# Kernel tuning notes

Hardware: AMD Instinct MI355X
Metric: run time of the kernel (lower is better)

The kernel has to match this reference:

```python
import jax, jax.numpy as jnp
import numpy as np

TEMPERATURE = 8.0  # sqrt(head_dim=64)
NEG_FILL = -1000000000.0

def setup_inputs() -> dict:
    key = jax.random.key(0)
    k1, k2, k3, k4, k5 = jax.random.split(key, 5)
    B, H, S, D = 4, 16, 1024, 64
    q = jax.random.normal(k1, (B, H, S, D), dtype=jnp.float32)
    k = jax.random.normal(k2, (B, H, S, D), dtype=jnp.float32)
    v = jax.random.normal(k3, (B, H, S, D), dtype=jnp.float32)
    similarity = jax.random.normal(k4, (B, H, S, S), dtype=jnp.float32)
    mask = jax.random.randint(k5, (B, 1, S, S), 0, 2).astype(bool)
    return {"q": q, "k": k, "v": v, "similarity": similarity, "mask": mask}

def reference(q, k, v, similarity, mask):
    # scores: [B,H,S,S] = (q/temp) @ k^T
    attn = jnp.einsum('bhqd,bhkd->bhqk', q / TEMPERATURE, k)
    attn = jnp.where(mask, NEG_FILL, attn)          # masked_fill (mask broadcasts over heads)
    attn = jax.nn.softmax(attn + similarity, axis=-1)  # dropout p=0 (eval): identity
    output = jnp.einsum('bhqk,bhkd->bhqd', attn, v)
    return (output, attn)
```

## Files before the change

### kernel.cpp

```cpp
#include <hip/hip_runtime.h>
#include <stdint.h>


#define S_LEN 1024
#define D_DIM 64
#define QT 16
#define NEG_FILL (-1000000000.0f)
#define LOG2E 1.44269504088896340736f

typedef __bf16 bf16x8 __attribute__((ext_vector_type(8)));
typedef float f32x4 __attribute__((ext_vector_type(4)));
typedef unsigned short u16x4 __attribute__((ext_vector_type(4)));

__device__ __forceinline__ unsigned short f2bf(float x) {
    unsigned u = __builtin_bit_cast(unsigned, x);
    u += 0x7fffu + ((u >> 16) & 1u);
    return (unsigned short)(u >> 16);
}
__device__ __forceinline__ float bf2f(unsigned short b) {
    return __builtin_bit_cast(float, (unsigned)b << 16);
}

__device__ __forceinline__ unsigned short* sptr(unsigned short* s, int row, int col) {
    return (unsigned short*)((char*)s + row * 2048 + ((col * 2) ^ ((row & 7) << 4)));
}

__global__ void prep_qkm(const float* __restrict__ q, const float* __restrict__ k,
                         const void* __restrict__ mraw,
                         unsigned short* __restrict__ Qb, unsigned short* __restrict__ Kb,
                         unsigned char* __restrict__ Mb)
{
    const int t = threadIdx.x;
    const int i = blockIdx.x * 256 + t;
    f32x4 q4 = ((const f32x4*)q)[i];
    f32x4 k4 = ((const f32x4*)k)[i];
    u16x4 qo, ko;
#pragma unroll
    for (int j = 0; j < 4; ++j) {
        qo[j] = f2bf(q4[j] * 0.125f);
        ko[j] = f2bf(k4[j]);
    }
    ((u16x4*)Qb)[i] = qo;
    ((u16x4*)Kb)[i] = ko;

    __shared__ int s_not_int, s_not_f32;
    if (t == 0) { s_not_int = 0; s_not_f32 = 0; }
    __syncthreads();
    const unsigned* wdd = (const unsigned*)mraw;
    int ni = 0, nf = 0;
    for (int j = t; j < 1024; j += 256) {
        unsigned x = wdd[j];
        if (x > 1u) ni = 1;
        if (x != 0u && x != 0x3f800000u) nf = 1;
    }
    if (ni) s_not_int = 1;
    if (nf) s_not_f32 = 1;
    __syncthreads();
    const int fmt = (s_not_int == 0) ? 0 : ((s_not_f32 == 0) ? 1 : 2);
    uchar4 o;
    if (fmt == 0) {
        int4 x = ((const int4*)mraw)[i];
        o.x = x.x ? 1 : 0; o.y = x.y ? 1 : 0; o.z = x.z ? 1 : 0; o.w = x.w ? 1 : 0;
    } else if (fmt == 1) {
        float4 x = ((const float4*)mraw)[i];
        o.x = (x.x != 0.f) ? 1 : 0; o.y = (x.y != 0.f) ? 1 : 0;
        o.z = (x.z != 0.f) ? 1 : 0; o.w = (x.w != 0.f) ? 1 : 0;
    } else {
        uchar4 x = ((const uchar4*)mraw)[i];
        o.x = x.x ? 1 : 0; o.y = x.y ? 1 : 0; o.z = x.z ? 1 : 0; o.w = x.w ? 1 : 0;
    }
    ((uchar4*)Mb)[i] = o;
}

__global__ void prep_vt(const float* __restrict__ v, unsigned short* __restrict__ Vt)
{
    __shared__ unsigned short sT[64 * 72];
    const int bh = blockIdx.x >> 4;
    const int st = blockIdx.x & 15;
    const int t = threadIdx.x;
    const float* vb = v + (size_t)(bh * S_LEN + st * 64) * D_DIM;
#pragma unroll
    for (int p = 0; p < 4; ++p) {
        int lin = p * 256 + t;
        int r = lin >> 4;
        int c = lin & 15;
        f32x4 x = ((const f32x4*)(vb + r * D_DIM))[c];
        unsigned short* dst = &sT[r * 72 + c * 4];
#pragma unroll
        for (int j = 0; j < 4; ++j) dst[j] = f2bf(x[j]);
    }
    __syncthreads();
    unsigned short* ob = Vt + (size_t)bh * D_DIM * S_LEN + st * 64;
#pragma unroll
    for (int p = 0; p < 4; ++p) {
        int lin = p * 256 + t;
        int d = lin >> 4;
        int s4 = (lin & 15) * 4;
        u16x4 o;
#pragma unroll
        for (int j = 0; j < 4; ++j) o[j] = sT[(s4 + j) * 72 + d];
        *(u16x4*)&ob[d * S_LEN + s4] = o;
    }
}

__global__ __launch_bounds__(256, 5)
void attn_main(const float* __restrict__ simg_, const unsigned short* __restrict__ Qb,
               const unsigned short* __restrict__ Kb, const unsigned short* __restrict__ Vtb,
               const unsigned char* __restrict__ Mb, float* __restrict__ out,
               float* __restrict__ attn)
{
    __shared__ __align__(16) unsigned short sS[QT * S_LEN];

    const int blk = blockIdx.x;
    const int bh = blk >> 6;
    const int qt = blk & 63;
    const int b = bh >> 4;
    const int t = threadIdx.x;
    const int w = t >> 6;
    const int lane = t & 63;
    const int quad = lane >> 4;
    const int l15 = lane & 15;

    const unsigned short* Qg = Qb + (size_t)(bh * S_LEN + qt * QT) * D_DIM;
    const unsigned short* Kg = Kb + (size_t)bh * S_LEN * D_DIM;
    const unsigned short* Vg = Vtb + (size_t)bh * D_DIM * S_LEN;
    const float* simg = simg_ + ((size_t)(bh * S_LEN + qt * QT)) * S_LEN;
    const unsigned char* mg = Mb + ((size_t)(b * S_LEN + qt * QT)) * S_LEN;
    float* attng = attn + ((size_t)(bh * S_LEN + qt * QT)) * S_LEN;

    const int n0 = w * 16;
    const bf16x8 av0 = *(const bf16x8*)&Qg[l15 * D_DIM + quad * 8];
    const bf16x8 av1 = *(const bf16x8*)&Qg[l15 * D_DIM + 32 + quad * 8];
    const unsigned short* kp0 = &Kg[(size_t)(n0 + l15) * D_DIM + quad * 8];
    bf16x8 kb0 = *(const bf16x8*)kp0;
    bf16x8 kb1 = *(const bf16x8*)(kp0 + 32);
#pragma unroll 4
    for (int kt = 0; kt < 16; ++kt) {
        bf16x8 bv0 = kb0, bv1 = kb1;
        if (kt < 15) {
            const unsigned short* kp = &Kg[(size_t)((kt + 1) * 64 + n0 + l15) * D_DIM + quad * 8];
            kb0 = *(const bf16x8*)kp;
            kb1 = *(const bf16x8*)(kp + 32);
        }
        f32x4 acc = {0.f, 0.f, 0.f, 0.f};
        acc = __builtin_amdgcn_mfma_f32_16x16x32_bf16(av0, bv0, acc, 0, 0, 0);
        acc = __builtin_amdgcn_mfma_f32_16x16x32_bf16(av1, bv1, acc, 0, 0, 0);
        const int colg = kt * 64 + n0 + l15;
#pragma unroll
        for (int r = 0; r < 4; ++r)
            *sptr(sS, quad * 4 + r, colg) = f2bf(acc[r]);
    }

    const float* sp_w = simg + (size_t)(w * 4) * S_LEN;
    f32x4 svb[2][4];
#pragma unroll
    for (int j = 0; j < 4; ++j)
        svb[0][j] = __builtin_nontemporal_load((const f32x4*)&sp_w[j * 256 + lane * 4]);
    __syncthreads();

#pragma unroll
    for (int rr = 0; rr < 4; ++rr) {
        const int cb = rr & 1;
        const int row = w * 4 + rr;
        if (rr < 3) {
            const float* spn = sp_w + (size_t)(rr + 1) * S_LEN;
#pragma unroll
            for (int j = 0; j < 4; ++j)
                svb[cb ^ 1][j] = __builtin_nontemporal_load((const f32x4*)&spn[j * 256 + lane * 4]);
        }
        const unsigned char* mp = mg + (size_t)row * S_LEN;
        float vals[16];
        float mx = -3.0e38f;
#pragma unroll
        for (int j = 0; j < 4; ++j) {
            const int col = j * 256 + lane * 4;
            u16x4 x = *(const u16x4*)sptr(sS, row, col);
            uchar4 mk = *(const uchar4*)&mp[col];
            f32x4 sv = svb[cb][j];
            float f0 = mk.x ? NEG_FILL : (bf2f(x[0]) + sv[0]);
            float f1 = mk.y ? NEG_FILL : (bf2f(x[1]) + sv[1]);
            float f2 = mk.z ? NEG_FILL : (bf2f(x[2]) + sv[2]);
            float f3 = mk.w ? NEG_FILL : (bf2f(x[3]) + sv[3]);
            vals[j * 4 + 0] = f0; vals[j * 4 + 1] = f1;
            vals[j * 4 + 2] = f2; vals[j * 4 + 3] = f3;
            mx = fmaxf(mx, fmaxf(fmaxf(f0, f1), fmaxf(f2, f3)));
        }
#pragma unroll
        for (int off = 32; off > 0; off >>= 1)
            mx = fmaxf(mx, __shfl_xor(mx, off, 64));
        float sum = 0.f;
#pragma unroll
        for (int i = 0; i < 16; ++i) {
            float e = __builtin_amdgcn_exp2f((vals[i] - mx) * LOG2E);
            vals[i] = e;
            sum += e;
        }
#pragma unroll
        for (int off = 32; off > 0; off >>= 1)
            sum += __shfl_xor(sum, off, 64);
        const float rinv = 1.0f / sum;
#pragma unroll
        for (int j = 0; j < 4; ++j) {
            const int col = j * 256 + lane * 4;
            f32x4 p;
            u16x4 pb;
#pragma unroll
            for (int i = 0; i < 4; ++i) {
                float pi = vals[j * 4 + i] * rinv;
                p[i] = pi;
                pb[i] = f2bf(pi);
            }
            __builtin_nontemporal_store(p, (f32x4*)&attng[(size_t)row * S_LEN + col]);
            *(u16x4*)sptr(sS, row, col) = pb;
        }
    }

    const int d0 = w * 16;
    const unsigned short* vpp = &Vg[(size_t)(d0 + l15) * S_LEN + quad * 8];
    bf16x8 vb0 = *(const bf16x8*)vpp;
    bf16x8 vb1 = *(const bf16x8*)(vpp + 32);
    __syncthreads();

    f32x4 oacc = {0.f, 0.f, 0.f, 0.f};
#pragma unroll 4
    for (int kt = 0; kt < 16; ++kt) {
        bf16x8 bv0 = vb0, bv1 = vb1;
        if (kt < 15) {
            const unsigned short* vp = &Vg[(size_t)(d0 + l15) * S_LEN + (kt + 1) * 64 + quad * 8];
            vb0 = *(const bf16x8*)vp;
            vb1 = *(const bf16x8*)(vp + 32);
        }
        bf16x8 pa0 = *(const bf16x8*)sptr(sS, l15, kt * 64 + quad * 8);
        bf16x8 pa1 = *(const bf16x8*)sptr(sS, l15, kt * 64 + 32 + quad * 8);
        oacc = __builtin_amdgcn_mfma_f32_16x16x32_bf16(pa0, bv0, oacc, 0, 0, 0);
        oacc = __builtin_amdgcn_mfma_f32_16x16x32_bf16(pa1, bv1, oacc, 0, 0, 0);
    }
    float* og = out + ((size_t)(bh * S_LEN + qt * QT)) * D_DIM;
#pragma unroll
    for (int r = 0; r < 4; ++r) {
        const int row = quad * 4 + r;
        __builtin_nontemporal_store(oacc[r], &og[row * D_DIM + d0 + l15]);
    }
}

extern "C" void kernel_launch(void* const* d_in, const int* in_sizes, int n_in,
                              void* d_out, int out_size, void* d_ws, size_t ws_size,
                              hipStream_t stream)
{
    const float* q = (const float*)d_in[0];
    const float* k = (const float*)d_in[1];
    const float* v = (const float*)d_in[2];
    const float* sim = (const float*)d_in[3];
    const void* mask = d_in[4];
    float* out = (float*)d_out;
    float* attn = out + (size_t)4 * 16 * 1024 * 64;

    char* ws = (char*)d_ws;
    unsigned short* Qb = (unsigned short*)(ws + (size_t)0);
    unsigned short* Kb = (unsigned short*)(ws + ((size_t)8 << 20));
    unsigned short* Vt = (unsigned short*)(ws + ((size_t)16 << 20));
    unsigned char*  Mb = (unsigned char*)(ws + ((size_t)24 << 20));

    prep_qkm<<<4096, 256, 0, stream>>>(q, k, mask, Qb, Kb, Mb);
    prep_vt<<<1024, 256, 0, stream>>>(v, Vt);
    attn_main<<<4096, 256, 0, stream>>>(sim, Qb, Kb, Vt, Mb, out, attn);
}
```

Measured before the change: 576.9 us.

## Deepen K/V prefetch, batch softmax rows in pairs, remap blocks across XCDs

```diff
diff --git a/kernel.cpp b/kernel.cpp
--- a/kernel.cpp
+++ b/kernel.cpp
@@ -103,7 +103,75 @@
     }
 }
 
-__global__ __launch_bounds__(256, 5)
+__device__ __forceinline__ void softmax2(
+    unsigned short* sS, const int row0, const int lane,
+    f32x4 (&v0)[4], f32x4 (&v1)[4],
+    uchar4 (&k0)[4], uchar4 (&k1)[4],
+    float* __restrict__ a0, float* __restrict__ a1)
+{
+    u16x4 x0[4], x1[4];
+#pragma unroll
+    for (int j = 0; j < 4; ++j) {
+        const int col = j * 256 + lane * 4;
+        x0[j] = *(const u16x4*)sptr(sS, row0, col);
+        x1[j] = *(const u16x4*)sptr(sS, row0 + 1, col);
+    }
+    float mx0 = -3.0e38f, mx1 = -3.0e38f;
+#pragma unroll
+    for (int j = 0; j < 4; ++j) {
+        f32x4 a = v0[j], b = v1[j];
+        const uchar4 ka = k0[j], kb = k1[j];
+        a[0] = ka.x ? NEG_FILL : (bf2f(x0[j][0]) + a[0]);
+        a[1] = ka.y ? NEG_FILL : (bf2f(x0[j][1]) + a[1]);
+        a[2] = ka.z ? NEG_FILL : (bf2f(x0[j][2]) + a[2]);
+        a[3] = ka.w ? NEG_FILL : (bf2f(x0[j][3]) + a[3]);
+        b[0] = kb.x ? NEG_FILL : (bf2f(x1[j][0]) + b[0]);
+        b[1] = kb.y ? NEG_FILL : (bf2f(x1[j][1]) + b[1]);
+        b[2] = kb.z ? NEG_FILL : (bf2f(x1[j][2]) + b[2]);
+        b[3] = kb.w ? NEG_FILL : (bf2f(x1[j][3]) + b[3]);
+        v0[j] = a; v1[j] = b;
+        mx0 = fmaxf(mx0, fmaxf(fmaxf(a[0], a[1]), fmaxf(a[2], a[3])));
+        mx1 = fmaxf(mx1, fmaxf(fmaxf(b[0], b[1]), fmaxf(b[2], b[3])));
+    }
+#pragma unroll
+    for (int off = 32; off > 0; off >>= 1) {
+        mx0 = fmaxf(mx0, __shfl_xor(mx0, off, 64));
+        mx1 = fmaxf(mx1, __shfl_xor(mx1, off, 64));
+    }
+    float s0 = 0.f, s1 = 0.f;
+#pragma unroll
+    for (int j = 0; j < 4; ++j) {
+        f32x4 a = v0[j], b = v1[j];
+#pragma unroll
+        for (int i = 0; i < 4; ++i) {
+            a[i] = __builtin_amdgcn_exp2f((a[i] - mx0) * LOG2E);
+            b[i] = __builtin_amdgcn_exp2f((b[i] - mx1) * LOG2E);
+            s0 += a[i];
+            s1 += b[i];
+        }
+        v0[j] = a; v1[j] = b;
+    }
+#pragma unroll
+    for (int off = 32; off > 0; off >>= 1) {
+        s0 += __shfl_xor(s0, off, 64);
+        s1 += __shfl_xor(s1, off, 64);
+    }
+    const float r0 = 1.0f / s0, r1 = 1.0f / s1;
+#pragma unroll
+    for (int j = 0; j < 4; ++j) {
+        const int col = j * 256 + lane * 4;
+        f32x4 p0 = v0[j] * r0, p1 = v1[j] * r1;
+        u16x4 q0, q1;
+#pragma unroll
+        for (int i = 0; i < 4; ++i) { q0[i] = f2bf(p0[i]); q1[i] = f2bf(p1[i]); }
+        __builtin_nontemporal_store(p0, (f32x4*)(a0 + col));
+        __builtin_nontemporal_store(p1, (f32x4*)(a1 + col));
+        *(u16x4*)sptr(sS, row0, col) = q0;
+        *(u16x4*)sptr(sS, row0 + 1, col) = q1;
+    }
+}
+
+__global__ __launch_bounds__(256, 4)
 void attn_main(const float* __restrict__ simg_, const unsigned short* __restrict__ Qb,
                const unsigned short* __restrict__ Kb, const unsigned short* __restrict__ Vtb,
                const unsigned char* __restrict__ Mb, float* __restrict__ out,
@@ -111,7 +179,7 @@
 {
     __shared__ __align__(16) unsigned short sS[QT * S_LEN];
 
-    const int blk = blockIdx.x;
+    const int blk = ((blockIdx.x & 7) << 9) | (blockIdx.x >> 3);
     const int bh = blk >> 6;
     const int qt = blk & 63;
     const int b = bh >> 4;
@@ -131,116 +199,119 @@
     const int n0 = w * 16;
     const bf16x8 av0 = *(const bf16x8*)&Qg[l15 * D_DIM + quad * 8];
     const bf16x8 av1 = *(const bf16x8*)&Qg[l15 * D_DIM + 32 + quad * 8];
-    const unsigned short* kp0 = &Kg[(size_t)(n0 + l15) * D_DIM + quad * 8];
-    bf16x8 kb0 = *(const bf16x8*)kp0;
-    bf16x8 kb1 = *(const bf16x8*)(kp0 + 32);
-#pragma unroll 4
-    for (int kt = 0; kt < 16; ++kt) {
-        bf16x8 bv0 = kb0, bv1 = kb1;
-        if (kt < 15) {
-            const unsigned short* kp = &Kg[(size_t)((kt + 1) * 64 + n0 + l15) * D_DIM + quad * 8];
-            kb0 = *(const bf16x8*)kp;
-            kb1 = *(const bf16x8*)(kp + 32);
-        }
-        f32x4 acc = {0.f, 0.f, 0.f, 0.f};
-        acc = __builtin_amdgcn_mfma_f32_16x16x32_bf16(av0, bv0, acc, 0, 0, 0);
-        acc = __builtin_amdgcn_mfma_f32_16x16x32_bf16(av1, bv1, acc, 0, 0, 0);
-        const int colg = kt * 64 + n0 + l15;
-#pragma unroll
-        for (int r = 0; r < 4; ++r)
-            *sptr(sS, quad * 4 + r, colg) = f2bf(acc[r]);
+    const unsigned short* kfrag = Kg + (size_t)(n0 + l15) * D_DIM + quad * 8;
+
+#define SB __builtin_amdgcn_sched_barrier(0)
+#define LOADK(D0, D1, KT) do { \
+    const unsigned short* _p = kfrag + (size_t)(KT) * 4096; \
+    D0 = *(const bf16x8*)_p; D1 = *(const bf16x8*)(_p + 32); } while (0)
+#define QKSTEP(F0, F1, KT) do { \
+    f32x4 _acc = {0.f, 0.f, 0.f, 0.f}; \
+    _acc = __builtin_amdgcn_mfma_f32_16x16x32_bf16(av0, F0, _acc, 0, 0, 0); \
+    _acc = __builtin_amdgcn_mfma_f32_16x16x32_bf16(av1, F1, _acc, 0, 0, 0); \
+    const int _cg = (KT) * 64 + n0 + l15; \
+    *sptr(sS, quad * 4 + 0, _cg) = f2bf(_acc[0]); \
+    *sptr(sS, quad * 4 + 1, _cg) = f2bf(_acc[1]); \
+    *sptr(sS, quad * 4 + 2, _cg) = f2bf(_acc[2]); \
+    *sptr(sS, quad * 4 + 3, _cg) = f2bf(_acc[3]); } while (0)
+
+    {
+        bf16x8 ka0, ka1, kb0, kb1, kc0, kc1, kd0, kd1;
+        LOADK(ka0, ka1, 0); LOADK(kb0, kb1, 1); LOADK(kc0, kc1, 2); LOADK(kd0, kd1, 3);
+        SB;
+        QKSTEP(ka0, ka1, 0);  LOADK(ka0, ka1, 4);  SB;
+        QKSTEP(kb0, kb1, 1);  LOADK(kb0, kb1, 5);  SB;
+        QKSTEP(kc0, kc1, 2);  LOADK(kc0, kc1, 6);  SB;
+        QKSTEP(kd0, kd1, 3);  LOADK(kd0, kd1, 7);  SB;
+        QKSTEP(ka0, ka1, 4);  LOADK(ka0, ka1, 8);  SB;
+        QKSTEP(kb0, kb1, 5);  LOADK(kb0, kb1, 9);  SB;
+        QKSTEP(kc0, kc1, 6);  LOADK(kc0, kc1, 10); SB;
+        QKSTEP(kd0, kd1, 7);  LOADK(kd0, kd1, 11); SB;
+        QKSTEP(ka0, ka1, 8);  LOADK(ka0, ka1, 12); SB;
+        QKSTEP(kb0, kb1, 9);  LOADK(kb0, kb1, 13); SB;
+        QKSTEP(kc0, kc1, 10); LOADK(kc0, kc1, 14); SB;
+        QKSTEP(kd0, kd1, 11); LOADK(kd0, kd1, 15); SB;
+        QKSTEP(ka0, ka1, 12);
+        QKSTEP(kb0, kb1, 13);
+        QKSTEP(kc0, kc1, 14);
+        QKSTEP(kd0, kd1, 15);
     }
 
     const float* sp_w = simg + (size_t)(w * 4) * S_LEN;
-    f32x4 svb[2][4];
-#pragma unroll
-    for (int j = 0; j < 4; ++j)
-        svb[0][j] = __builtin_nontemporal_load((const f32x4*)&sp_w[j * 256 + lane * 4]);
-    __syncthreads();
-
-#pragma unroll
-    for (int rr = 0; rr < 4; ++rr) {
-        const int cb = rr & 1;
-        const int row = w * 4 + rr;
-        if (rr < 3) {
-            const float* spn = sp_w + (size_t)(rr + 1) * S_LEN;
-#pragma unroll
-            for (int j = 0; j < 4; ++j)
-                svb[cb ^ 1][j] = __builtin_nontemporal_load((const f32x4*)&spn[j * 256 + lane * 4]);
-        }
-        const unsigned char* mp = mg + (size_t)row * S_LEN;
-        float vals[16];
-        float mx = -3.0e38f;
-#pragma unroll
-        for (int j = 0; j < 4; ++j) {
-            const int col = j * 256 + lane * 4;
-            u16x4 x = *(const u16x4*)sptr(sS, row, col);
-            uchar4 mk = *(const uchar4*)&mp[col];
-            f32x4 sv = svb[cb][j];
-            float f0 = mk.x ? NEG_FILL : (bf2f(x[0]) + sv[0]);
-            float f1 = mk.y ? NEG_FILL : (bf2f(x[1]) + sv[1]);
-            float f2 = mk.z ? NEG_FILL : (bf2f(x[2]) + sv[2]);
-            float f3 = mk.w ? NEG_FILL : (bf2f(x[3]) + sv[3]);
-            vals[j * 4 + 0] = f0; vals[j * 4 + 1] = f1;
-            vals[j * 4 + 2] = f2; vals[j * 4 + 3] = f3;
-            mx = fmaxf(mx, fmaxf(fmaxf(f0, f1), fmaxf(f2, f3)));
-        }
-#pragma unroll
-        for (int off = 32; off > 0; off >>= 1)
-            mx = fmaxf(mx, __shfl_xor(mx, off, 64));
-        float sum = 0.f;
-#pragma unroll
-        for (int i = 0; i < 16; ++i) {
-            float e = __builtin_amdgcn_exp2f((vals[i] - mx) * LOG2E);
-            vals[i] = e;
-            sum += e;
-        }
-#pragma unroll
-        for (int off = 32; off > 0; off >>= 1)
-            sum += __shfl_xor(sum, off, 64);
-        const float rinv = 1.0f / sum;
-#pragma unroll
-        for (int j = 0; j < 4; ++j) {
-            const int col = j * 256 + lane * 4;
-            f32x4 p;
-            u16x4 pb;
-#pragma unroll
-            for (int i = 0; i < 4; ++i) {
-                float pi = vals[j * 4 + i] * rinv;
-                p[i] = pi;
-                pb[i] = f2bf(pi);
-            }
-            __builtin_nontemporal_store(p, (f32x4*)&attng[(size_t)row * S_LEN + col]);
-            *(u16x4*)sptr(sS, row, col) = pb;
-        }
-    }
+    const unsigned char* mp_w = mg + (size_t)(w * 4) * S_LEN;
+    f32x4 sA[4], sB[4], sC[4], sD[4];
+    uchar4 mA[4], mB[4], mC[4], mD[4];
+#pragma unroll
+    for (int j = 0; j < 4; ++j) {
+        const int col = j * 256 + lane * 4;
+        sA[j] = __builtin_nontemporal_load((const f32x4*)&sp_w[col]);
+        sB[j] = __builtin_nontemporal_load((const f32x4*)&sp_w[S_LEN + col]);
+        mA[j] = *(const uchar4*)&mp_w[col];
+        mB[j] = *(const uchar4*)&mp_w[S_LEN + col];
+    }
+    SB;
+    __syncthreads();
+
+#pragma unroll
+    for (int j = 0; j < 4; ++j) {
+        const int col = j * 256 + lane * 4;
+        sC[j] = __builtin_nontemporal_load((const f32x4*)&sp_w[2 * S_LEN + col]);
+        sD[j] = __builtin_nontemporal_load((const f32x4*)&sp_w[3 * S_LEN + col]);
+        mC[j] = *(const uchar4*)&mp_w[2 * S_LEN + col];
+        mD[j] = *(const uchar4*)&mp_w[3 * S_LEN + col];
+    }
+    SB;
+    softmax2(sS, w * 4 + 0, lane, sA, sB, mA, mB,
+             attng + (size_t)(w * 4 + 0) * S_LEN, attng + (size_t)(w * 4 + 1) * S_LEN);
+    softmax2(sS, w * 4 + 2, lane, sC, sD, mC, mD,
+             attng + (size_t)(w * 4 + 2) * S_LEN, attng + (size_t)(w * 4 + 3) * S_LEN);
 
     const int d0 = w * 16;
-    const unsigned short* vpp = &Vg[(size_t)(d0 + l15) * S_LEN + quad * 8];
-    bf16x8 vb0 = *(const bf16x8*)vpp;
-    bf16x8 vb1 = *(const bf16x8*)(vpp + 32);
+    const unsigned short* vfrag = Vg + (size_t)(d0 + l15) * S_LEN + quad * 8;
+
+#define LOADV(D0, D1, KT) do { \
+    const unsigned short* _p = vfrag + (KT) * 64; \
+    D0 = *(const bf16x8*)_p; D1 = *(const bf16x8*)(_p + 32); } while (0)
+#define PVSTEP(F0, F1, KT) do { \
+    bf16x8 _pa0 = *(const bf16x8*)sptr(sS, l15, (KT) * 64 + quad * 8); \
+    bf16x8 _pa1 = *(const bf16x8*)sptr(sS, l15, (KT) * 64 + 32 + quad * 8); \
+    oacc = __builtin_amdgcn_mfma_f32_16x16x32_bf16(_pa0, F0, oacc, 0, 0, 0); \
+    oacc = __builtin_amdgcn_mfma_f32_16x16x32_bf16(_pa1, F1, oacc, 0, 0, 0); } while (0)
+
+    bf16x8 va0, va1, vb0, vb1, vc0, vc1, vd0, vd1;
+    LOADV(va0, va1, 0); LOADV(vb0, vb1, 1); LOADV(vc0, vc1, 2); LOADV(vd0, vd1, 3);
+    SB;
     __syncthreads();
 
     f32x4 oacc = {0.f, 0.f, 0.f, 0.f};
-#pragma unroll 4
-    for (int kt = 0; kt < 16; ++kt) {
-        bf16x8 bv0 = vb0, bv1 = vb1;
-        if (kt < 15) {
-            const unsigned short* vp = &Vg[(size_t)(d0 + l15) * S_LEN + (kt + 1) * 64 + quad * 8];
-            vb0 = *(const bf16x8*)vp;
-            vb1 = *(const bf16x8*)(vp + 32);
-        }
-        bf16x8 pa0 = *(const bf16x8*)sptr(sS, l15, kt * 64 + quad * 8);
-        bf16x8 pa1 = *(const bf16x8*)sptr(sS, l15, kt * 64 + 32 + quad * 8);
-        oacc = __builtin_amdgcn_mfma_f32_16x16x32_bf16(pa0, bv0, oacc, 0, 0, 0);
-        oacc = __builtin_amdgcn_mfma_f32_16x16x32_bf16(pa1, bv1, oacc, 0, 0, 0);
-    }
+    PVSTEP(va0, va1, 0);  LOADV(va0, va1, 4);  SB;
+    PVSTEP(vb0, vb1, 1);  LOADV(vb0, vb1, 5);  SB;
+    PVSTEP(vc0, vc1, 2);  LOADV(vc0, vc1, 6);  SB;
+    PVSTEP(vd0, vd1, 3);  LOADV(vd0, vd1, 7);  SB;
+    PVSTEP(va0, va1, 4);  LOADV(va0, va1, 8);  SB;
+    PVSTEP(vb0, vb1, 5);  LOADV(vb0, vb1, 9);  SB;
+    PVSTEP(vc0, vc1, 6);  LOADV(vc0, vc1, 10); SB;
+    PVSTEP(vd0, vd1, 7);  LOADV(vd0, vd1, 11); SB;
+    PVSTEP(va0, va1, 8);  LOADV(va0, va1, 12); SB;
+    PVSTEP(vb0, vb1, 9);  LOADV(vb0, vb1, 13); SB;
+    PVSTEP(vc0, vc1, 10); LOADV(vc0, vc1, 14); SB;
+    PVSTEP(vd0, vd1, 11); LOADV(vd0, vd1, 15); SB;
+    PVSTEP(va0, va1, 12);
+    PVSTEP(vb0, vb1, 13);
+    PVSTEP(vc0, vc1, 14);
+    PVSTEP(vd0, vd1, 15);
+
     float* og = out + ((size_t)(bh * S_LEN + qt * QT)) * D_DIM;
 #pragma unroll
     for (int r = 0; r < 4; ++r) {
         const int row = quad * 4 + r;
         __builtin_nontemporal_store(oacc[r], &og[row * D_DIM + d0 + l15]);
     }
+#undef SB
+#undef LOADK
+#undef QKSTEP
+#undef LOADV
+#undef PVSTEP
 }
 
 extern "C" void kernel_launch(void* const* d_in, const int* in_sizes, int n_in,
```

Result: no change. 570.5 us (-1.1%).

## Pipeline K/V loads four deep with explicit vmcnt waits and swizzle block order

Applied to the files above, without the earlier changes.

```diff
diff --git a/kernel.cpp b/kernel.cpp
--- a/kernel.cpp
+++ b/kernel.cpp
@@ -20,6 +20,20 @@
 __device__ __forceinline__ float bf2f(unsigned short b) {
     return __builtin_bit_cast(float, (unsigned)b << 16);
 }
+
+__device__ __forceinline__ f32x4 gload16(const void* p) {
+    f32x4 d;
+    asm volatile("global_load_dwordx4 %0, %1, off" : "=v"(d) : "v"(p) : "memory");
+    return d;
+}
+__device__ __forceinline__ unsigned gload4(const void* p) {
+    unsigned d;
+    asm volatile("global_load_dword %0, %1, off" : "=v"(d) : "v"(p) : "memory");
+    return d;
+}
+#define WAITV(N) do { \
+    asm volatile("s_waitcnt vmcnt(" #N ")" ::: "memory"); \
+    __builtin_amdgcn_sched_barrier(0); } while (0)
 
 __device__ __forceinline__ unsigned short* sptr(unsigned short* s, int row, int col) {
     return (unsigned short*)((char*)s + row * 2048 + ((col * 2) ^ ((row & 7) << 4)));
@@ -103,7 +117,7 @@
     }
 }
 
-__global__ __launch_bounds__(256, 5)
+__global__ __launch_bounds__(256, 4)
 void attn_main(const float* __restrict__ simg_, const unsigned short* __restrict__ Qb,
                const unsigned short* __restrict__ Kb, const unsigned short* __restrict__ Vtb,
                const unsigned char* __restrict__ Mb, float* __restrict__ out,
@@ -111,7 +125,7 @@
 {
     __shared__ __align__(16) unsigned short sS[QT * S_LEN];
 
-    const int blk = blockIdx.x;
+    const int blk = ((blockIdx.x & 7) << 9) | (blockIdx.x >> 3);
     const int bh = blk >> 6;
     const int qt = blk & 63;
     const int b = bh >> 4;
@@ -120,6 +134,7 @@
     const int lane = t & 63;
     const int quad = lane >> 4;
     const int l15 = lane & 15;
+    const int n0 = w * 16;
 
     const unsigned short* Qg = Qb + (size_t)(bh * S_LEN + qt * QT) * D_DIM;
     const unsigned short* Kg = Kb + (size_t)bh * S_LEN * D_DIM;
@@ -128,59 +143,74 @@
     const unsigned char* mg = Mb + ((size_t)(b * S_LEN + qt * QT)) * S_LEN;
     float* attng = attn + ((size_t)(bh * S_LEN + qt * QT)) * S_LEN;
 
-    const int n0 = w * 16;
     const bf16x8 av0 = *(const bf16x8*)&Qg[l15 * D_DIM + quad * 8];
     const bf16x8 av1 = *(const bf16x8*)&Qg[l15 * D_DIM + 32 + quad * 8];
-    const unsigned short* kp0 = &Kg[(size_t)(n0 + l15) * D_DIM + quad * 8];
-    bf16x8 kb0 = *(const bf16x8*)kp0;
-    bf16x8 kb1 = *(const bf16x8*)(kp0 + 32);
-#pragma unroll 4
-    for (int kt = 0; kt < 16; ++kt) {
-        bf16x8 bv0 = kb0, bv1 = kb1;
-        if (kt < 15) {
-            const unsigned short* kp = &Kg[(size_t)((kt + 1) * 64 + n0 + l15) * D_DIM + quad * 8];
-            kb0 = *(const bf16x8*)kp;
-            kb1 = *(const bf16x8*)(kp + 32);
-        }
-        f32x4 acc = {0.f, 0.f, 0.f, 0.f};
-        acc = __builtin_amdgcn_mfma_f32_16x16x32_bf16(av0, bv0, acc, 0, 0, 0);
-        acc = __builtin_amdgcn_mfma_f32_16x16x32_bf16(av1, bv1, acc, 0, 0, 0);
-        const int colg = kt * 64 + n0 + l15;
-#pragma unroll
-        for (int r = 0; r < 4; ++r)
-            *sptr(sS, quad * 4 + r, colg) = f2bf(acc[r]);
+    const unsigned short* kfrag = Kg + (size_t)(n0 + l15) * D_DIM + quad * 8;
+
+#define KLOAD(D0, D1, KT) do { \
+    D0 = __builtin_bit_cast(bf16x8, gload16(kfrag + (size_t)(KT) * 4096)); \
+    D1 = __builtin_bit_cast(bf16x8, gload16(kfrag + (size_t)(KT) * 4096 + 32)); } while (0)
+#define QKSTEP(F0, F1, KT) do { \
+    f32x4 _acc = {0.f, 0.f, 0.f, 0.f}; \
+    _acc = __builtin_amdgcn_mfma_f32_16x16x32_bf16(av0, F0, _acc, 0, 0, 0); \
+    _acc = __builtin_amdgcn_mfma_f32_16x16x32_bf16(av1, F1, _acc, 0, 0, 0); \
+    const int _cg = (KT) * 64 + n0 + l15; \
+    *sptr(sS, quad * 4 + 0, _cg) = f2bf(_acc[0]); \
+    *sptr(sS, quad * 4 + 1, _cg) = f2bf(_acc[1]); \
+    *sptr(sS, quad * 4 + 2, _cg) = f2bf(_acc[2]); \
+    *sptr(sS, quad * 4 + 3, _cg) = f2bf(_acc[3]); } while (0)
+
+    {
+        bf16x8 ka0, ka1, kb0, kb1, kc0, kc1, kd0, kd1;
+        KLOAD(ka0, ka1, 0); KLOAD(kb0, kb1, 1); KLOAD(kc0, kc1, 2); KLOAD(kd0, kd1, 3);
+        WAITV(6);  QKSTEP(ka0, ka1, 0);  KLOAD(ka0, ka1, 4);
+        WAITV(6);  QKSTEP(kb0, kb1, 1);  KLOAD(kb0, kb1, 5);
+        WAITV(6);  QKSTEP(kc0, kc1, 2);  KLOAD(kc0, kc1, 6);
+        WAITV(6);  QKSTEP(kd0, kd1, 3);  KLOAD(kd0, kd1, 7);
+        WAITV(6);  QKSTEP(ka0, ka1, 4);  KLOAD(ka0, ka1, 8);
+        WAITV(6);  QKSTEP(kb0, kb1, 5);  KLOAD(kb0, kb1, 9);
+        WAITV(6);  QKSTEP(kc0, kc1, 6);  KLOAD(kc0, kc1, 10);
+        WAITV(6);  QKSTEP(kd0, kd1, 7);  KLOAD(kd0, kd1, 11);
+        WAITV(6);  QKSTEP(ka0, ka1, 8);  KLOAD(ka0, ka1, 12);
+        WAITV(6);  QKSTEP(kb0, kb1, 9);  KLOAD(kb0, kb1, 13);
+        WAITV(6);  QKSTEP(kc0, kc1, 10); KLOAD(kc0, kc1, 14);
+        WAITV(6);  QKSTEP(kd0, kd1, 11); KLOAD(kd0, kd1, 15);
+        WAITV(6);  QKSTEP(ka0, ka1, 12);
+        WAITV(4);  QKSTEP(kb0, kb1, 13);
+        WAITV(2);  QKSTEP(kc0, kc1, 14);
+        WAITV(0);  QKSTEP(kd0, kd1, 15);
     }
 
     const float* sp_w = simg + (size_t)(w * 4) * S_LEN;
-    f32x4 svb[2][4];
-#pragma unroll
-    for (int j = 0; j < 4; ++j)
-        svb[0][j] = __builtin_nontemporal_load((const f32x4*)&sp_w[j * 256 + lane * 4]);
-    __syncthreads();
+    const unsigned char* mp_w = mg + (size_t)(w * 4) * S_LEN;
+    f32x4 sv[4][4];
+    unsigned mv[4][4];
+#pragma unroll
+    for (int rr = 0; rr < 4; ++rr)
+#pragma unroll
+        for (int j = 0; j < 4; ++j) {
+            const int col = j * 256 + lane * 4;
+            sv[rr][j] = gload16(sp_w + (size_t)rr * S_LEN + col);
+            mv[rr][j] = gload4(mp_w + (size_t)rr * S_LEN + col);
+        }
+    __syncthreads();
+    WAITV(0);
 
 #pragma unroll
     for (int rr = 0; rr < 4; ++rr) {
-        const int cb = rr & 1;
         const int row = w * 4 + rr;
-        if (rr < 3) {
-            const float* spn = sp_w + (size_t)(rr + 1) * S_LEN;
-#pragma unroll
-            for (int j = 0; j < 4; ++j)
-                svb[cb ^ 1][j] = __builtin_nontemporal_load((const f32x4*)&spn[j * 256 + lane * 4]);
-        }
-        const unsigned char* mp = mg + (size_t)row * S_LEN;
         float vals[16];
         float mx = -3.0e38f;
 #pragma unroll
         for (int j = 0; j < 4; ++j) {
             const int col = j * 256 + lane * 4;
             u16x4 x = *(const u16x4*)sptr(sS, row, col);
-            uchar4 mk = *(const uchar4*)&mp[col];
-            f32x4 sv = svb[cb][j];
-            float f0 = mk.x ? NEG_FILL : (bf2f(x[0]) + sv[0]);
-            float f1 = mk.y ? NEG_FILL : (bf2f(x[1]) + sv[1]);
-            float f2 = mk.z ? NEG_FILL : (bf2f(x[2]) + sv[2]);
-            float f3 = mk.w ? NEG_FILL : (bf2f(x[3]) + sv[3]);
+            const unsigned m = mv[rr][j];
+            const f32x4 s = sv[rr][j];
+            float f0 = (m & 0x000000ffu) ? NEG_FILL : (bf2f(x[0]) + s[0]);
+            float f1 = (m & 0x0000ff00u) ? NEG_FILL : (bf2f(x[1]) + s[1]);
+            float f2 = (m & 0x00ff0000u) ? NEG_FILL : (bf2f(x[2]) + s[2]);
+            float f3 = (m & 0xff000000u) ? NEG_FILL : (bf2f(x[3]) + s[3]);
             vals[j * 4 + 0] = f0; vals[j * 4 + 1] = f1;
             vals[j * 4 + 2] = f2; vals[j * 4 + 3] = f3;
             mx = fmaxf(mx, fmaxf(fmaxf(f0, f1), fmaxf(f2, f3)));
@@ -202,45 +232,68 @@
 #pragma unroll
         for (int j = 0; j < 4; ++j) {
             const int col = j * 256 + lane * 4;
-            f32x4 p;
             u16x4 pb;
 #pragma unroll
-            for (int i = 0; i < 4; ++i) {
-                float pi = vals[j * 4 + i] * rinv;
-                p[i] = pi;
-                pb[i] = f2bf(pi);
-            }
+            for (int i = 0; i < 4; ++i)
+                pb[i] = f2bf(vals[j * 4 + i] * rinv);
+            *(u16x4*)sptr(sS, row, col) = pb;
+        }
+    }
+
+    const int d0 = w * 16;
+    const unsigned short* vfrag = Vg + (size_t)(d0 + l15) * S_LEN + quad * 8;
+
+#define VLOAD(D0, D1, KT) do { \
+    D0 = __builtin_bit_cast(bf16x8, gload16(vfrag + (KT) * 64)); \
+    D1 = __builtin_bit_cast(bf16x8, gload16(vfrag + (KT) * 64 + 32)); } while (0)
+#define PVSTEP(F0, F1, KT) do { \
+    bf16x8 _pa0 = *(const bf16x8*)sptr(sS, l15, (KT) * 64 + quad * 8); \
+    bf16x8 _pa1 = *(const bf16x8*)sptr(sS, l15, (KT) * 64 + 32 + quad * 8); \
+    oacc = __builtin_amdgcn_mfma_f32_16x16x32_bf16(_pa0, F0, oacc, 0, 0, 0); \
+    oacc = __builtin_amdgcn_mfma_f32_16x16x32_bf16(_pa1, F1, oacc, 0, 0, 0); } while (0)
+
+    bf16x8 va0, va1, vb0, vb1, vc0, vc1, vd0, vd1;
+    VLOAD(va0, va1, 0); VLOAD(vb0, vb1, 1); VLOAD(vc0, vc1, 2); VLOAD(vd0, vd1, 3);
+    __syncthreads();
+
+    f32x4 oacc = {0.f, 0.f, 0.f, 0.f};
+    WAITV(6);  PVSTEP(va0, va1, 0);  VLOAD(va0, va1, 4);
+    WAITV(6);  PVSTEP(vb0, vb1, 1);  VLOAD(vb0, vb1, 5);
+    WAITV(6);  PVSTEP(vc0, vc1, 2);  VLOAD(vc0, vc1, 6);
+    WAITV(6);  PVSTEP(vd0, vd1, 3);  VLOAD(vd0, vd1, 7);
+    WAITV(6);  PVSTEP(va0, va1, 4);  VLOAD(va0, va1, 8);
+    WAITV(6);  PVSTEP(vb0, vb1, 5);  VLOAD(vb0, vb1, 9);
+    WAITV(6);  PVSTEP(vc0, vc1, 6);  VLOAD(vc0, vc1, 10);
+    WAITV(6);  PVSTEP(vd0, vd1, 7);  VLOAD(vd0, vd1, 11);
+    WAITV(6);  PVSTEP(va0, va1, 8);  VLOAD(va0, va1, 12);
+    WAITV(6);  PVSTEP(vb0, vb1, 9);  VLOAD(vb0, vb1, 13);
+    WAITV(6);  PVSTEP(vc0, vc1, 10); VLOAD(vc0, vc1, 14);
+    WAITV(6);  PVSTEP(vd0, vd1, 11); VLOAD(vd0, vd1, 15);
+    WAITV(6);  PVSTEP(va0, va1, 12);
+    WAITV(4);  PVSTEP(vb0, vb1, 13);
+    WAITV(2);  PVSTEP(vc0, vc1, 14);
+    WAITV(0);  PVSTEP(vd0, vd1, 15);
+
+    float* og = out + ((size_t)(bh * S_LEN + qt * QT)) * D_DIM;
+#pragma unroll
+    for (int r = 0; r < 4; ++r)
+        __builtin_nontemporal_store(oacc[r], &og[(quad * 4 + r) * D_DIM + d0 + l15]);
+
+#pragma unroll
+    for (int rr = 0; rr < 4; ++rr) {
+        const int row = w * 4 + rr;
+#pragma unroll
+        for (int j = 0; j < 4; ++j) {
+            const int col = j * 256 + lane * 4;
+            u16x4 x = *(const u16x4*)sptr(sS, row, col);
+            f32x4 p = { bf2f(x[0]), bf2f(x[1]), bf2f(x[2]), bf2f(x[3]) };
             __builtin_nontemporal_store(p, (f32x4*)&attng[(size_t)row * S_LEN + col]);
-            *(u16x4*)sptr(sS, row, col) = pb;
-        }
-    }
-
-    const int d0 = w * 16;
-    const unsigned short* vpp = &Vg[(size_t)(d0 + l15) * S_LEN + quad * 8];
-    bf16x8 vb0 = *(const bf16x8*)vpp;
-    bf16x8 vb1 = *(const bf16x8*)(vpp + 32);
-    __syncthreads();
-
-    f32x4 oacc = {0.f, 0.f, 0.f, 0.f};
-#pragma unroll 4
-    for (int kt = 0; kt < 16; ++kt) {
-        bf16x8 bv0 = vb0, bv1 = vb1;
-        if (kt < 15) {
-            const unsigned short* vp = &Vg[(size_t)(d0 + l15) * S_LEN + (kt + 1) * 64 + quad * 8];
-            vb0 = *(const bf16x8*)vp;
-            vb1 = *(const bf16x8*)(vp + 32);
-        }
-        bf16x8 pa0 = *(const bf16x8*)sptr(sS, l15, kt * 64 + quad * 8);
-        bf16x8 pa1 = *(const bf16x8*)sptr(sS, l15, kt * 64 + 32 + quad * 8);
-        oacc = __builtin_amdgcn_mfma_f32_16x16x32_bf16(pa0, bv0, oacc, 0, 0, 0);
-        oacc = __builtin_amdgcn_mfma_f32_16x16x32_bf16(pa1, bv1, oacc, 0, 0, 0);
-    }
-    float* og = out + ((size_t)(bh * S_LEN + qt * QT)) * D_DIM;
-#pragma unroll
-    for (int r = 0; r < 4; ++r) {
-        const int row = quad * 4 + r;
-        __builtin_nontemporal_store(oacc[r], &og[row * D_DIM + d0 + l15]);
-    }
+        }
+    }
+#undef KLOAD
+#undef QKSTEP
+#undef VLOAD
+#undef PVSTEP
 }
 
 extern "C" void kernel_launch(void* const* d_in, const int* in_sizes, int n_in,
```

After: 576.7 us. No clear change (-0.0%).
